# Kernel optimization log

Measured on AMD Instinct MI355X. Metric: run time of the kernel, lower is better.

Reference implementation:

```python
import jax, jax.numpy as jnp
import numpy as np

OUT_FEATURES = 16384
IN_FEATURES = 4096


def setup_inputs() -> dict:
    key = jax.random.key(0)
    k1, k2, k3, k4 = jax.random.split(key, 4)
    # activations [B, S, in]
    x = jax.random.normal(k1, (4, 2048, IN_FEATURES), dtype=jnp.float32)
    # packed int4 weights: two nibbles per uint8, total out*in values (even, no pad)
    n_packed = OUT_FEATURES * IN_FEATURES // 2
    weight_packed = jax.random.randint(k2, (n_packed,), 0, 256, dtype=jnp.int32).astype(jnp.uint8)
    # per-row dequant scale [out, 1], positive like abs-max/7
    scale = jax.random.uniform(k3, (OUT_FEATURES, 1), dtype=jnp.float32, minval=1e-3, maxval=0.05)
    bias = jax.random.normal(k4, (OUT_FEATURES,), dtype=jnp.float32) * 0.01
    return {"x": x, "weight_packed": weight_packed, "scale": scale, "bias": bias}


def reference(x, weight_packed, scale, bias):
    # unpack: even positions = low nibble, odd positions = high nibble
    low = (weight_packed & 15).astype(jnp.int8)
    high = ((weight_packed >> 4) & 15).astype(jnp.int8)
    q = jnp.stack([low, high], axis=-1).reshape(-1)  # interleave -> [out*in]
    # sign-extend 4-bit two's complement: values >7 map to negative
    q = jnp.where(q > 7, q - 16, q)
    # dequantize with per-row scale -> [out, in]
    w = q.reshape(OUT_FEATURES, IN_FEATURES).astype(jnp.float32) * scale
    # F.linear: y = x @ w.T + bias
    return jnp.einsum('bsi,oi->bso', x, w) + bias
```

## Files before the change

### kernel.cpp

```cpp
#include <hip/hip_runtime.h>
#include <hip/hip_bf16.h>
#include <stdint.h>

typedef short short8 __attribute__((ext_vector_type(8)));
typedef float floatx4 __attribute__((ext_vector_type(4)));

static constexpr int KTOT = 4096;
static constexpr int NTOT = 16384;
static constexpr int MTOT = 8192;

#define GLOAD_LDS16(g, l)                                              \
  __builtin_amdgcn_global_load_lds(                                    \
      (const __attribute__((address_space(1))) void*)(g),              \
      (__attribute__((address_space(3))) void*)(l), 16, 0, 0)

__device__ __forceinline__ uint32_t pack2_bf16_rne(float lo, float hi) {
  uint32_t a = __builtin_bit_cast(uint32_t, lo);
  uint32_t b = __builtin_bit_cast(uint32_t, hi);
  a += 0x7FFFu + ((a >> 16) & 1u);
  b += 0x7FFFu + ((b >> 16) & 1u);
  return __builtin_amdgcn_perm(b, a, 0x07060302u);
}


__global__ __launch_bounds__(256) void cvt_x_kernel(
    const float* __restrict__ X, ushort* __restrict__ Xb) {
  const size_t i = (size_t)blockIdx.x * 256 + threadIdx.x;
  const float4 a = *reinterpret_cast<const float4*>(X + i * 8);
  const float4 b = *reinterpret_cast<const float4*>(X + i * 8 + 4);
  uint4 o;
  o.x = pack2_bf16_rne(a.x, a.y);
  o.y = pack2_bf16_rne(a.z, a.w);
  o.z = pack2_bf16_rne(b.x, b.y);
  o.w = pack2_bf16_rne(b.z, b.w);
  *reinterpret_cast<uint4*>(Xb + i * 8) = o;
}

__global__ __launch_bounds__(256) void cvt_w_kernel(
    const uint32_t* __restrict__ Wp, ushort* __restrict__ Wb) {
  const size_t i = (size_t)blockIdx.x * 256 + threadIdx.x;
  const uint4 w = *reinterpret_cast<const uint4*>(Wp + i * 4);
  const uint32_t wd[4] = {w.x, w.y, w.z, w.w};
  uint4 o;
  uint32_t* op = reinterpret_cast<uint32_t*>(&o);
  #pragma unroll
  for (int p = 0; p < 4; ++p) {
    int v0 = ((int)(wd[p] << 28)) >> 28;
    int v1 = ((int)(wd[p] << 24)) >> 28;
    uint32_t f0 = __builtin_bit_cast(uint32_t, (float)v0);
    uint32_t f1 = __builtin_bit_cast(uint32_t, (float)v1);
    op[p] = __builtin_amdgcn_perm(f1, f0, 0x07060302u);
  }
  *reinterpret_cast<uint4*>(Wb + i * 8) = o;
}


static constexpr int BM = 256, BN = 256, BK = 32;
static constexpr int NT = KTOT / BK;

__global__ __launch_bounds__(512, 2) void gemm_bf16_256_kernel(
    const ushort* __restrict__ Xb,
    const ushort* __restrict__ Wb,
    const float* __restrict__ scale,
    const float* __restrict__ bias,
    float* __restrict__ Y)
{
  __shared__ ushort As[4 * 8192];
  __shared__ ushort Bs[4 * 8192];

  const int t    = threadIdx.x;
  const int lane = t & 63;
  const int wv   = t >> 6;
  const int wr   = wv >> 2;
  const int wcn  = wv & 3;

  const int wg  = blockIdx.x;
  const int xcd = wg & 7;
  const int s   = wg >> 3;
  const int bm0 = (xcd * 4 + (s & 3)) * BM;
  const int bn0 = (s >> 2) * BN;

  const int srow = wv * 16 + (lane >> 2);
  const int scol = 8 * ((lane & 3) ^ ((lane >> 2) & 3) ^ (lane >> 4));
  const ushort* agA = Xb + (size_t)(bm0 + srow) * KTOT + scol;
  const ushort* agB = Wb + (size_t)(bn0 + srow) * KTOT + scol;
  const size_t rowstep = (size_t)128 * KTOT;
  ushort* aldsw = As + wv * 512;
  ushort* bldsw = Bs + wv * 512;

  const int rcol = 8 * ((lane >> 4) ^ (lane & 3) ^ ((lane >> 2) & 3));
  const ushort* Abase = As + (wr * 128 + (lane & 15)) * 32 + rcol;
  const ushort* Bbase = Bs + (wcn * 64 + (lane & 15)) * 32 + rcol;

  floatx4 acc[8][4];
  #pragma unroll
  for (int m = 0; m < 8; ++m)
    #pragma unroll
    for (int n = 0; n < 4; ++n)
      acc[m][n] = (floatx4){0.f, 0.f, 0.f, 0.f};

  #pragma unroll
  for (int pt = 0; pt < 3; ++pt) {
    const size_t kof = (size_t)pt * BK;
    GLOAD_LDS16(agA + kof,           aldsw + pt * 8192);
    GLOAD_LDS16(agA + kof + rowstep, aldsw + pt * 8192 + 4096);
    GLOAD_LDS16(agB + kof,           bldsw + pt * 8192);
    GLOAD_LDS16(agB + kof + rowstep, bldsw + pt * 8192 + 4096);
  }
  asm volatile("s_waitcnt vmcnt(8)" ::: "memory");
  __builtin_amdgcn_s_barrier();

  for (int kt = 0; kt < NT; ++kt) {
    const int c  = kt & 3;
    const ushort* Ab = Abase + c * 8192;
    const ushort* Bb = Bbase + c * 8192;
    const int st = kt + 3;
    const bool do_stage = (st < NT);
    const int sb = st & 3;
    const size_t kof = (size_t)st * BK;

    short8 bf[4], af[4];
    #pragma unroll
    for (int n = 0; n < 4; ++n)
      bf[n] = *reinterpret_cast<const short8*>(Bb + n * 512);
    #pragma unroll
    for (int m = 0; m < 4; ++m)
      af[m] = *reinterpret_cast<const short8*>(Ab + m * 512);
    if (do_stage) {
      GLOAD_LDS16(agA + kof,           aldsw + sb * 8192);
      GLOAD_LDS16(agA + kof + rowstep, aldsw + sb * 8192 + 4096);
    }
    __builtin_amdgcn_s_barrier();
    asm volatile("s_waitcnt lgkmcnt(0)" ::: "memory");
    __builtin_amdgcn_sched_barrier(0);
    __builtin_amdgcn_s_setprio(1);
    #pragma unroll
    for (int m = 0; m < 4; ++m)
      #pragma unroll
      for (int n = 0; n < 4; ++n)
        acc[m][n] = __builtin_amdgcn_mfma_f32_16x16x32_bf16(af[m], bf[n], acc[m][n], 0, 0, 0);
    __builtin_amdgcn_s_setprio(0);
    __builtin_amdgcn_s_barrier();

    #pragma unroll
    for (int m = 0; m < 4; ++m)
      af[m] = *reinterpret_cast<const short8*>(Ab + (m + 4) * 512);
    if (do_stage) {
      GLOAD_LDS16(agB + kof,           bldsw + sb * 8192);
      GLOAD_LDS16(agB + kof + rowstep, bldsw + sb * 8192 + 4096);
    }
    __builtin_amdgcn_s_barrier();
    asm volatile("s_waitcnt lgkmcnt(0)" ::: "memory");
    __builtin_amdgcn_sched_barrier(0);
    __builtin_amdgcn_s_setprio(1);
    #pragma unroll
    for (int m = 0; m < 4; ++m)
      #pragma unroll
      for (int n = 0; n < 4; ++n)
        acc[m + 4][n] = __builtin_amdgcn_mfma_f32_16x16x32_bf16(af[m], bf[n], acc[m + 4][n], 0, 0, 0);
    __builtin_amdgcn_s_setprio(0);

    if (kt + 1 < NT) {
      if (kt + 4 <= NT)      { asm volatile("s_waitcnt vmcnt(8)" ::: "memory"); }
      else if (kt + 3 <= NT) { asm volatile("s_waitcnt vmcnt(4)" ::: "memory"); }
      else                   { asm volatile("s_waitcnt vmcnt(0)" ::: "memory"); }
      __builtin_amdgcn_s_barrier();
    }
  }

  const int crow = (lane >> 4) * 4;
  const int ccol = lane & 15;
  #pragma unroll
  for (int n = 0; n < 4; ++n) {
    const int col  = bn0 + wcn * 64 + n * 16 + ccol;
    const float sc = scale[col];
    const float bz = bias[col];
    #pragma unroll
    for (int m = 0; m < 8; ++m) {
      const int row0 = bm0 + wr * 128 + m * 16 + crow;
      float* yp = Y + (size_t)row0 * NTOT + col;
      #pragma unroll
      for (int r = 0; r < 4; ++r)
        yp[(size_t)r * NTOT] = acc[m][n][r] * sc + bz;
    }
  }
}


static constexpr int FBM = 128, FBN = 128, FBK = 64;
static constexpr int LDSS = 72;
static constexpr int FNSTEP = KTOT / FBK;

__global__ __launch_bounds__(256) void int4_linear_fused_kernel(
    const float* __restrict__ X,
    const uint32_t* __restrict__ Wp,
    const float* __restrict__ scale,
    const float* __restrict__ bias,
    float* __restrict__ Y)
{
  __shared__ ushort As[FBM * LDSS];
  __shared__ ushort Bs[FBN * LDSS];

  const int t    = threadIdx.x;
  const int lane = t & 63;
  const int wv   = t >> 6;
  const int wr   = wv >> 1;
  const int wc   = wv & 1;
  const int bm0 = blockIdx.y * FBM;
  const int bn0 = blockIdx.x * FBN;
  const int srow = t >> 1;
  const int sh   = t & 1;

  const float*    ag = X  + (size_t)(bm0 + srow) * KTOT + sh * 32;
  const uint32_t* bg = Wp + (size_t)(bn0 + srow) * (KTOT / 2) + sh * 16;

  float4 areg[8];
  uint4  breg[4];
  #pragma unroll
  for (int j = 0; j < 8; ++j) areg[j] = *reinterpret_cast<const float4*>(ag + j * 4);
  #pragma unroll
  for (int j = 0; j < 4; ++j) breg[j] = *reinterpret_cast<const uint4*>(bg + j * 4);

  floatx4 acc[4][4];
  #pragma unroll
  for (int m = 0; m < 4; ++m)
    #pragma unroll
    for (int n = 0; n < 4; ++n)
      acc[m][n] = (floatx4){0.f, 0.f, 0.f, 0.f};

  ushort* adst = &As[srow * LDSS + sh * 32];
  ushort* bdst = &Bs[srow * LDSS + sh * 32];

  for (int ks = 0; ks < FNSTEP; ++ks) {
    {
      uint32_t ab[16];
      #pragma unroll
      for (int j = 0; j < 8; ++j) {
        uint32_t u0 = __builtin_bit_cast(uint32_t, areg[j].x) + 0x8000u;
        uint32_t u1 = __builtin_bit_cast(uint32_t, areg[j].y) + 0x8000u;
        uint32_t u2 = __builtin_bit_cast(uint32_t, areg[j].z) + 0x8000u;
        uint32_t u3 = __builtin_bit_cast(uint32_t, areg[j].w) + 0x8000u;
        ab[2*j]   = __builtin_amdgcn_perm(u1, u0, 0x07060302u);
        ab[2*j+1] = __builtin_amdgcn_perm(u3, u2, 0x07060302u);
      }
      uint32_t bb[16];
      #pragma unroll
      for (int j = 0; j < 4; ++j) {
        const uint32_t wq[4] = {breg[j].x, breg[j].y, breg[j].z, breg[j].w};
        #pragma unroll
        for (int p = 0; p < 4; ++p) {
          const uint32_t w = wq[p];
          int v0 = ((int)(w << 28)) >> 28;
          int v1 = ((int)(w << 24)) >> 28;
          uint32_t f0 = __builtin_bit_cast(uint32_t, (float)v0);
          uint32_t f1 = __builtin_bit_cast(uint32_t, (float)v1);
          bb[j*4 + p] = __builtin_amdgcn_perm(f1, f0, 0x07060302u);
        }
      }
      #pragma unroll
      for (int j = 0; j < 4; ++j) {
        *reinterpret_cast<uint4*>(adst + j * 8) = *reinterpret_cast<const uint4*>(&ab[j*4]);
        *reinterpret_cast<uint4*>(bdst + j * 8) = *reinterpret_cast<const uint4*>(&bb[j*4]);
      }
    }
    __syncthreads();

    if (ks + 1 < FNSTEP) {
      const float*    ap = ag + (ks + 1) * FBK;
      const uint32_t* bp = bg + (ks + 1) * (FBK / 2);
      #pragma unroll
      for (int j = 0; j < 8; ++j) areg[j] = *reinterpret_cast<const float4*>(ap + j * 4);
      #pragma unroll
      for (int j = 0; j < 4; ++j) breg[j] = *reinterpret_cast<const uint4*>(bp + j * 4);
    }

    #pragma unroll
    for (int kk = 0; kk < 2; ++kk) {
      const int ko = kk * 32 + (lane >> 4) * 8;
      short8 af[4], bf[4];
      #pragma unroll
      for (int m = 0; m < 4; ++m)
        af[m] = *reinterpret_cast<const short8*>(&As[(wr*64 + m*16 + (lane & 15)) * LDSS + ko]);
      #pragma unroll
      for (int n = 0; n < 4; ++n)
        bf[n] = *reinterpret_cast<const short8*>(&Bs[(wc*64 + n*16 + (lane & 15)) * LDSS + ko]);
      #pragma unroll
      for (int m = 0; m < 4; ++m)
        #pragma unroll
        for (int n = 0; n < 4; ++n)
          acc[m][n] = __builtin_amdgcn_mfma_f32_16x16x32_bf16(af[m], bf[n], acc[m][n], 0, 0, 0);
    }
    __syncthreads();
  }

  const int crow = (lane >> 4) * 4;
  const int ccol = lane & 15;
  #pragma unroll
  for (int n = 0; n < 4; ++n) {
    const int col  = bn0 + wc * 64 + n * 16 + ccol;
    const float s  = scale[col];
    const float bz = bias[col];
    #pragma unroll
    for (int m = 0; m < 4; ++m) {
      const int row0 = bm0 + wr * 64 + m * 16 + crow;
      float* yp = Y + (size_t)row0 * NTOT + col;
      #pragma unroll
      for (int r = 0; r < 4; ++r)
        yp[(size_t)r * NTOT] = acc[m][n][r] * s + bz;
    }
  }
}


extern "C" void kernel_launch(void* const* d_in, const int* in_sizes, int n_in,
                              void* d_out, int out_size, void* d_ws, size_t ws_size,
                              hipStream_t stream) {
  (void)in_sizes; (void)n_in; (void)out_size;
  const float*    X     = (const float*)d_in[0];
  const uint32_t* Wp    = (const uint32_t*)d_in[1];
  const float*    scale = (const float*)d_in[2];
  const float*    bias  = (const float*)d_in[3];
  float*          Y     = (float*)d_out;

  const size_t xb_bytes = (size_t)MTOT * KTOT * 2;
  const size_t wb_bytes = (size_t)NTOT * KTOT * 2;
  if (ws_size >= xb_bytes + wb_bytes) {
    ushort* Xb = (ushort*)d_ws;
    ushort* Wb = (ushort*)((char*)d_ws + xb_bytes);
    cvt_x_kernel<<<(MTOT * KTOT) / (8 * 256), 256, 0, stream>>>(X, Xb);
    cvt_w_kernel<<<(NTOT * KTOT / 2) / (4 * 256), 256, 0, stream>>>(Wp, Wb);
    gemm_bf16_256_kernel<<<(MTOT / BM) * (NTOT / BN), 512, 0, stream>>>(Xb, Wb, scale, bias, Y);
  } else {
    dim3 grid(NTOT / FBN, MTOT / FBM);
    int4_linear_fused_kernel<<<grid, 256, 0, stream>>>(X, Wp, scale, bias, Y);
  }
}
```

Measured before the change: 1.282 ms.

## Merge two half-step phases into one per k-tile, dropping intra-iteration barriers

Result: faster. 1.182 ms (-7.8%).

```diff
diff --git a/kernel.cpp b/kernel.cpp
--- a/kernel.cpp
+++ b/kernel.cpp
@@ -107,8 +107,7 @@
     GLOAD_LDS16(agB + kof,           bldsw + pt * 8192);
     GLOAD_LDS16(agB + kof + rowstep, bldsw + pt * 8192 + 4096);
   }
-  asm volatile("s_waitcnt vmcnt(8)" ::: "memory");
-  __builtin_amdgcn_s_barrier();
+  asm volatile("s_waitcnt vmcnt(8)\ns_barrier" ::: "memory");
 
   for (int kt = 0; kt < NT; ++kt) {
     const int c  = kt & 3;
@@ -119,52 +118,41 @@
     const int sb = st & 3;
     const size_t kof = (size_t)st * BK;
 
-    short8 bf[4], af[4];
+    short8 bf[4], af0[4], af1[4];
     #pragma unroll
     for (int n = 0; n < 4; ++n)
       bf[n] = *reinterpret_cast<const short8*>(Bb + n * 512);
     #pragma unroll
     for (int m = 0; m < 4; ++m)
-      af[m] = *reinterpret_cast<const short8*>(Ab + m * 512);
+      af0[m] = *reinterpret_cast<const short8*>(Ab + m * 512);
+    #pragma unroll
+    for (int m = 0; m < 4; ++m)
+      af1[m] = *reinterpret_cast<const short8*>(Ab + (m + 4) * 512);
+
     if (do_stage) {
       GLOAD_LDS16(agA + kof,           aldsw + sb * 8192);
       GLOAD_LDS16(agA + kof + rowstep, aldsw + sb * 8192 + 4096);
-    }
-    __builtin_amdgcn_s_barrier();
-    asm volatile("s_waitcnt lgkmcnt(0)" ::: "memory");
-    __builtin_amdgcn_sched_barrier(0);
-    __builtin_amdgcn_s_setprio(1);
-    #pragma unroll
-    for (int m = 0; m < 4; ++m)
-      #pragma unroll
-      for (int n = 0; n < 4; ++n)
-        acc[m][n] = __builtin_amdgcn_mfma_f32_16x16x32_bf16(af[m], bf[n], acc[m][n], 0, 0, 0);
-    __builtin_amdgcn_s_setprio(0);
-    __builtin_amdgcn_s_barrier();
-
-    #pragma unroll
-    for (int m = 0; m < 4; ++m)
-      af[m] = *reinterpret_cast<const short8*>(Ab + (m + 4) * 512);
-    if (do_stage) {
       GLOAD_LDS16(agB + kof,           bldsw + sb * 8192);
       GLOAD_LDS16(agB + kof + rowstep, bldsw + sb * 8192 + 4096);
     }
-    __builtin_amdgcn_s_barrier();
-    asm volatile("s_waitcnt lgkmcnt(0)" ::: "memory");
-    __builtin_amdgcn_sched_barrier(0);
+
     __builtin_amdgcn_s_setprio(1);
     #pragma unroll
     for (int m = 0; m < 4; ++m)
       #pragma unroll
       for (int n = 0; n < 4; ++n)
-        acc[m + 4][n] = __builtin_amdgcn_mfma_f32_16x16x32_bf16(af[m], bf[n], acc[m + 4][n], 0, 0, 0);
+        acc[m][n] = __builtin_amdgcn_mfma_f32_16x16x32_bf16(af0[m], bf[n], acc[m][n], 0, 0, 0);
+    #pragma unroll
+    for (int m = 0; m < 4; ++m)
+      #pragma unroll
+      for (int n = 0; n < 4; ++n)
+        acc[m + 4][n] = __builtin_amdgcn_mfma_f32_16x16x32_bf16(af1[m], bf[n], acc[m + 4][n], 0, 0, 0);
     __builtin_amdgcn_s_setprio(0);
 
     if (kt + 1 < NT) {
-      if (kt + 4 <= NT)      { asm volatile("s_waitcnt vmcnt(8)" ::: "memory"); }
-      else if (kt + 3 <= NT) { asm volatile("s_waitcnt vmcnt(4)" ::: "memory"); }
-      else                   { asm volatile("s_waitcnt vmcnt(0)" ::: "memory"); }
-      __builtin_amdgcn_s_barrier();
+      if (kt + 4 <= NT)      { asm volatile("s_waitcnt vmcnt(8)\ns_barrier" ::: "memory"); }
+      else if (kt + 3 <= NT) { asm volatile("s_waitcnt vmcnt(4)\ns_barrier" ::: "memory"); }
+      else                   { asm volatile("s_waitcnt vmcnt(0)\ns_barrier" ::: "memory"); }
     }
   }
 
```
